# Kernel optimization log

Measured on AMD Instinct MI355X. Metric: run time of the kernel, lower is better.

## Reference

```python
import jax, jax.numpy as jnp
import numpy as np

EPSILON = 0.001
PROXIMITY_THRESHOLD = 0.15


def setup_inputs() -> dict:
    key = jax.random.key(0)
    k1, k2, k3 = jax.random.split(key, 3)
    B, N, E = 8, 512, 4096
    node_positions = jax.random.uniform(k1, (B, N, 2), dtype=jnp.float32)
    adjacency = jax.random.normal(k2, (B, N, N), dtype=jnp.float32)
    edge_index = jax.random.randint(k3, (2, E), 0, B * N, dtype=jnp.int64)
    return {"node_positions": node_positions, "adjacency": adjacency, "edge_index": edge_index}


def _candidate_mask(pos, src, dst, batch, prox):
    # pos: (BN,2); src/dst/batch: (E,)
    p_src = pos[src]
    p_dst = pos[dst]
    mid = (p_src + p_dst) * 0.5                      # (E,2)
    half = jnp.linalg.norm(p_dst - p_src, axis=-1) * 0.5  # (E,)
    dist = jnp.linalg.norm(mid[:, None] - mid[None, :], axis=-1)  # (E,E)
    reach = half[:, None] + half[None, :] + prox
    E = src.shape[0]
    idx = jnp.arange(E)
    upper = idx[None, :] > idx[:, None]              # ei < ej
    same_batch = batch[:, None] == batch[None, :]
    shares = ((src[:, None] == src[None, :]) | (src[:, None] == dst[None, :])
              | (dst[:, None] == src[None, :]) | (dst[:, None] == dst[None, :]))
    return (dist < reach) & upper & same_batch & ~shares


def _segment_distance_dense(p_src, p_dst):
    # All-pairs closest-approach distance between segments i and j.
    d1 = p_dst - p_src                               # (E,2)
    sq = jnp.maximum((d1 * d1).sum(-1), 1e-12)       # (E,)
    a = sq[:, None]                                  # a_i
    e = sq[None, :]                                  # e_j
    b = d1 @ d1.T                                    # (E,E) d1_i . d1_j
    d1_dot_a1 = (d1 * p_src).sum(-1)                 # (E,) d1_k . a1_k
    c = d1_dot_a1[:, None] - d1 @ p_src.T            # d1_i . (a1_i - b1_j)
    f = p_src @ d1.T - d1_dot_a1[None, :]            # d1_j . (a1_i - b1_j)
    denom = jnp.maximum(a * e - b * b, 1e-12)
    s = (b * f - c * e) / denom
    t = (a * f - b * c) / denom
    s = jnp.clip(s, 0.0, 1.0)
    t = jnp.clip(t, 0.0, 1.0)
    t = jnp.clip((b * s + f) / e, 0.0, 1.0)
    s = jnp.clip((b * t - c) / a, 0.0, 1.0)
    closest_a = p_src[:, None, :] + s[..., None] * d1[:, None, :]   # (E,E,2)
    closest_b = p_src[None, :, :] + t[..., None] * d1[None, :, :]   # (E,E,2)
    return jnp.linalg.norm(closest_a - closest_b, axis=-1)          # (E,E)


def reference(node_positions, adjacency, edge_index):
    # adjacency is accepted (per the torch forward signature) but unused by this axiom.
    B, N, _ = node_positions.shape
    pos = node_positions.reshape(-1, 2)              # (B*N, 2)
    src = edge_index[0]
    dst = edge_index[1]
    batch = src // N                                 # (E,) batch membership per edge
    mask = jax.lax.stop_gradient(
        _candidate_mask(jax.lax.stop_gradient(pos), src, dst, batch, PROXIMITY_THRESHOLD))
    dmin = _segment_distance_dense(pos[src], pos[dst])  # (E,E)
    pair_loss = jax.nn.relu(EPSILON - dmin) * mask.astype(dmin.dtype)
    n_pairs = mask.sum()
    loss = pair_loss.sum() / jnp.maximum(n_pairs, 1).astype(dmin.dtype)
    violation_mask = mask & (pair_loss > 0)
    violation_scores = jax.lax.stop_gradient(pair_loss)
    return loss, violation_mask, violation_scores
```

## Files before the change

### kernel.cpp

```cpp
#include <hip/hip_runtime.h>


#define EDGES   4096
#define LOGE    12
#define EPS     0.001f
#define PROX    0.15f
#define NBUCKET 2048

__global__ __launch_bounds__(256) void pair_kernel(
    const float2* __restrict__ pos,
    const int*    __restrict__ esrc,
    const int*    __restrict__ edst,
    float*        __restrict__ out,
    float*        __restrict__ bsum,
    unsigned int* __restrict__ bcnt)
{
#pragma clang fp contract(off)
    const int k = blockIdx.x * 256 + threadIdx.x;
    const int i = k >> LOGE;
    const int j = k & (EDGES - 1);

    const int si = esrc[i], di = edst[i];
    const int sj = esrc[j], dj = edst[j];
    const float2 a1 = pos[si], a2 = pos[di];
    const float2 b1 = pos[sj], b2 = pos[dj];

    const float d1ix = a2.x - a1.x, d1iy = a2.y - a1.y;
    const float d1jx = b2.x - b1.x, d1jy = b2.y - b1.y;
    const float midix = (a1.x + a2.x) * 0.5f, midiy = (a1.y + a2.y) * 0.5f;
    const float midjx = (b1.x + b2.x) * 0.5f, midjy = (b1.y + b2.y) * 0.5f;
    const float half_i = sqrtf(d1ix * d1ix + d1iy * d1iy) * 0.5f;
    const float half_j = sqrtf(d1jx * d1jx + d1jy * d1jy) * 0.5f;
    const float dmx = midix - midjx, dmy = midiy - midjy;
    const float dist  = sqrtf(dmx * dmx + dmy * dmy);
    const float reach = half_i + half_j + PROX;

    const bool upper  = j > i;
    const bool sameb  = (si >> 9) == (sj >> 9);
    const bool shares = (si == sj) || (si == dj) || (di == sj) || (di == dj);
    const bool mask   = (dist < reach) && upper && sameb && !shares;

    const float sqi = fmaxf(d1ix * d1ix + d1iy * d1iy, 1e-12f);
    const float sqj = fmaxf(d1jx * d1jx + d1jy * d1jy, 1e-12f);
    const float b   = d1ix * d1jx + d1iy * d1jy;
    const float ddai = d1ix * a1.x + d1iy * a1.y;
    const float ddaj = d1jx * b1.x + d1jy * b1.y;
    const float c = ddai - (d1ix * b1.x + d1iy * b1.y);
    const float f = (a1.x * d1jx + a1.y * d1jy) - ddaj;
    const float denom = fmaxf(sqi * sqj - b * b, 1e-12f);

    float s = (b * f - c * sqj) / denom;
    s = fminf(fmaxf(s, 0.0f), 1.0f);
    const float t = fminf(fmaxf((b * s + f) / sqj, 0.0f), 1.0f);
    s = fminf(fmaxf((b * t - c) / sqi, 0.0f), 1.0f);

    const float cax = a1.x + s * d1ix, cay = a1.y + s * d1iy;
    const float cbx = b1.x + t * d1jx, cby = b1.y + t * d1jy;
    const float dx = cax - cbx, dy = cay - cby;
    const float dmin = sqrtf(dx * dx + dy * dy);

    const float mf = mask ? 1.0f : 0.0f;
    const float pl = fmaxf(EPS - dmin, 0.0f) * mf;

    out[1 + k] = (mask && pl > 0.0f) ? 1.0f : 0.0f;
    out[1 + EDGES * EDGES + k] = pl;

    float vsum = pl;
    int   vcnt = mask ? 1 : 0;
    #pragma unroll
    for (int off = 32; off > 0; off >>= 1) {
        vsum += __shfl_xor(vsum, off, 64);
        vcnt += __shfl_xor(vcnt, off, 64);
    }
    __shared__ float    ls[4];
    __shared__ unsigned lc[4];
    const int wid = threadIdx.x >> 6, lane = threadIdx.x & 63;
    if (lane == 0) { ls[wid] = vsum; lc[wid] = (unsigned)vcnt; }
    __syncthreads();
    if (threadIdx.x == 0) {
        const float    s4 = ls[0] + ls[1] + ls[2] + ls[3];
        const unsigned c4 = lc[0] + lc[1] + lc[2] + lc[3];
        const int bk = blockIdx.x & (NBUCKET - 1);
        atomicAdd(&bsum[bk], s4);
        atomicAdd(&bcnt[bk], c4);
    }
}

__global__ __launch_bounds__(256) void finalize_kernel(
    const float* __restrict__ bsum, const unsigned* __restrict__ bcnt,
    float* __restrict__ out)
{
    float    s = 0.0f;
    unsigned c = 0u;
    for (int b = threadIdx.x; b < NBUCKET; b += 256) { s += bsum[b]; c += bcnt[b]; }
    #pragma unroll
    for (int off = 32; off > 0; off >>= 1) {
        s += __shfl_xor(s, off, 64);
        c += (unsigned)__shfl_xor((int)c, off, 64);
    }
    __shared__ float    ls[4];
    __shared__ unsigned lc[4];
    const int wid = threadIdx.x >> 6, lane = threadIdx.x & 63;
    if (lane == 0) { ls[wid] = s; lc[wid] = c; }
    __syncthreads();
    if (threadIdx.x == 0) {
        const float    st = ls[0] + ls[1] + ls[2] + ls[3];
        const unsigned ct = lc[0] + lc[1] + lc[2] + lc[3];
        const unsigned n  = ct > 1u ? ct : 1u;
        out[0] = st / (float)n;
    }
}

extern "C" void kernel_launch(void* const* d_in, const int* in_sizes, int n_in,
                              void* d_out, int out_size, void* d_ws, size_t ws_size,
                              hipStream_t stream) {
    const float2* pos  = (const float2*)d_in[0];
    const int*    esrc = (const int*)d_in[2];
    const int*    edst = esrc + EDGES;

    float*        out  = (float*)d_out;
    float*        bsum = (float*)d_ws;
    unsigned int* bcnt = (unsigned int*)((float*)d_ws + NBUCKET);

    hipMemsetAsync(d_ws, 0, NBUCKET * 2 * sizeof(float), stream);

    const int nPairs = EDGES * EDGES;
    pair_kernel<<<nPairs / 256, 256, 0, stream>>>(pos, esrc, edst, out, bsum, bcnt);
    finalize_kernel<<<1, 256, 0, stream>>>(bsum, bcnt, out);
}
```

Measured before the change: 214.9 us.

## Precompute per-edge records and skip lower-triangle pair blocks early

Adds an edge_pre kernel that computes each edge's direction, midpoint, half-length, squared length and dot terms once and packs them into three float4 records. The pair kernel then reads these records instead of doing indirect gathers through edge_index and recomputing per-edge quantities. Blocks that lie entirely in the lower triangle (j <= i) write zeros and return early, and blocks whose partial sum and count are zero skip their atomics. This trades an extra small launch and workspace traffic for much less per-pair arithmetic and gather work. The kernel still has to write the two large output arrays, which likely bounds how much time can be saved.

```diff
diff --git a/kernel.cpp b/kernel.cpp
--- a/kernel.cpp
+++ b/kernel.cpp
@@ -7,46 +7,67 @@
 #define PROX    0.15f
 #define NBUCKET 2048
 
-__global__ __launch_bounds__(256) void pair_kernel(
+__global__ __launch_bounds__(256) void edge_pre(
     const float2* __restrict__ pos,
     const int*    __restrict__ esrc,
     const int*    __restrict__ edst,
+    float4* __restrict__ rec1, float4* __restrict__ rec2, float4* __restrict__ rec3)
+{
+#pragma clang fp contract(off)
+    const int e = blockIdx.x * 256 + threadIdx.x;
+    const int s = esrc[e], d = edst[e];
+    const float2 a1 = pos[s], a2 = pos[d];
+    const float d1x = a2.x - a1.x, d1y = a2.y - a1.y;
+    const float midx = (a1.x + a2.x) * 0.5f, midy = (a1.y + a2.y) * 0.5f;
+    const float half = sqrtf(d1x * d1x + d1y * d1y) * 0.5f;
+    const float sq   = fmaxf(d1x * d1x + d1y * d1y, 1e-12f);
+    const float dda  = d1x * a1.x + d1y * a1.y;
+    rec1[e] = make_float4(a1.x, a1.y, d1x, d1y);
+    rec2[e] = make_float4(midx, midy, half, dda);
+    rec3[e] = make_float4(sq, __int_as_float(s), __int_as_float(d), 0.0f);
+}
+
+__global__ __launch_bounds__(256) void pair_kernel(
+    const float4* __restrict__ rec1, const float4* __restrict__ rec2,
+    const float4* __restrict__ rec3,
     float*        __restrict__ out,
     float*        __restrict__ bsum,
     unsigned int* __restrict__ bcnt)
 {
 #pragma clang fp contract(off)
-    const int k = blockIdx.x * 256 + threadIdx.x;
-    const int i = k >> LOGE;
-    const int j = k & (EDGES - 1);
+    const int bi    = blockIdx.x;
+    const int i     = bi >> 4;
+    const int jbase = (bi & 15) << 8;
+    const int j     = jbase + threadIdx.x;
+    const int k     = (i << LOGE) | j;
 
-    const int si = esrc[i], di = edst[i];
-    const int sj = esrc[j], dj = edst[j];
-    const float2 a1 = pos[si], a2 = pos[di];
-    const float2 b1 = pos[sj], b2 = pos[dj];
+    float* __restrict__ o_mask  = out + 1;
+    float* __restrict__ o_score = out + 1 + EDGES * EDGES;
 
-    const float d1ix = a2.x - a1.x, d1iy = a2.y - a1.y;
-    const float d1jx = b2.x - b1.x, d1jy = b2.y - b1.y;
-    const float midix = (a1.x + a2.x) * 0.5f, midiy = (a1.y + a2.y) * 0.5f;
-    const float midjx = (b1.x + b2.x) * 0.5f, midjy = (b1.y + b2.y) * 0.5f;
-    const float half_i = sqrtf(d1ix * d1ix + d1iy * d1iy) * 0.5f;
-    const float half_j = sqrtf(d1jx * d1jx + d1jy * d1jy) * 0.5f;
-    const float dmx = midix - midjx, dmy = midiy - midjy;
-    const float dist  = sqrtf(dmx * dmx + dmy * dmy);
-    const float reach = half_i + half_j + PROX;
+    if (jbase + 255 <= i) {
+        o_mask[k]  = 0.0f;
+        o_score[k] = 0.0f;
+        return;
+    }
 
+    const float4 r1i = rec1[i], r2i = rec2[i], r3i = rec3[i];
+    const float4 r1j = rec1[j], r2j = rec2[j], r3j = rec3[j];
+
+    const float dmx  = r2i.x - r2j.x, dmy = r2i.y - r2j.y;
+    const float dist = sqrtf(dmx * dmx + dmy * dmy);
+    const float reach = r2i.z + r2j.z + PROX;
+
+    const int si = __float_as_int(r3i.y), di_ = __float_as_int(r3i.z);
+    const int sj = __float_as_int(r3j.y), dj  = __float_as_int(r3j.z);
     const bool upper  = j > i;
     const bool sameb  = (si >> 9) == (sj >> 9);
-    const bool shares = (si == sj) || (si == dj) || (di == sj) || (di == dj);
-    const bool mask   = (dist < reach) && upper && sameb && !shares;
+    const bool shares = (si == sj) | (si == dj) | (di_ == sj) | (di_ == dj);
+    const bool mask   = (dist < reach) & upper & sameb & (!shares);
 
-    const float sqi = fmaxf(d1ix * d1ix + d1iy * d1iy, 1e-12f);
-    const float sqj = fmaxf(d1jx * d1jx + d1jy * d1jy, 1e-12f);
-    const float b   = d1ix * d1jx + d1iy * d1jy;
-    const float ddai = d1ix * a1.x + d1iy * a1.y;
-    const float ddaj = d1jx * b1.x + d1jy * b1.y;
-    const float c = ddai - (d1ix * b1.x + d1iy * b1.y);
-    const float f = (a1.x * d1jx + a1.y * d1jy) - ddaj;
+    const float sqi = r3i.x, sqj = r3j.x;
+    const float b = r1i.z * r1j.z + r1i.w * r1j.w;
+    const float c = r2i.w - (r1i.z * r1j.x + r1i.w * r1j.y);
+    const float f = (r1i.x * r1j.z + r1i.y * r1j.w) - r2j.w;
     const float denom = fmaxf(sqi * sqj - b * b, 1e-12f);
 
     float s = (b * f - c * sqj) / denom;
@@ -54,16 +75,15 @@
     const float t = fminf(fmaxf((b * s + f) / sqj, 0.0f), 1.0f);
     s = fminf(fmaxf((b * t - c) / sqi, 0.0f), 1.0f);
 
-    const float cax = a1.x + s * d1ix, cay = a1.y + s * d1iy;
-    const float cbx = b1.x + t * d1jx, cby = b1.y + t * d1jy;
+    const float cax = r1i.x + s * r1i.z, cay = r1i.y + s * r1i.w;
+    const float cbx = r1j.x + t * r1j.z, cby = r1j.y + t * r1j.w;
     const float dx = cax - cbx, dy = cay - cby;
     const float dmin = sqrtf(dx * dx + dy * dy);
 
-    const float mf = mask ? 1.0f : 0.0f;
-    const float pl = fmaxf(EPS - dmin, 0.0f) * mf;
+    const float pl = fmaxf(EPS - dmin, 0.0f) * (mask ? 1.0f : 0.0f);
 
-    out[1 + k] = (mask && pl > 0.0f) ? 1.0f : 0.0f;
-    out[1 + EDGES * EDGES + k] = pl;
+    o_mask[k]  = (mask && pl > 0.0f) ? 1.0f : 0.0f;
+    o_score[k] = pl;
 
     float vsum = pl;
     int   vcnt = mask ? 1 : 0;
@@ -80,9 +100,11 @@
     if (threadIdx.x == 0) {
         const float    s4 = ls[0] + ls[1] + ls[2] + ls[3];
         const unsigned c4 = lc[0] + lc[1] + lc[2] + lc[3];
-        const int bk = blockIdx.x & (NBUCKET - 1);
-        atomicAdd(&bsum[bk], s4);
-        atomicAdd(&bcnt[bk], c4);
+        if (s4 != 0.0f || c4 != 0u) {
+            const int bk = blockIdx.x & (NBUCKET - 1);
+            atomicAdd(&bsum[bk], s4);
+            atomicAdd(&bcnt[bk], c4);
+        }
     }
 }
 
@@ -121,10 +143,13 @@
     float*        out  = (float*)d_out;
     float*        bsum = (float*)d_ws;
     unsigned int* bcnt = (unsigned int*)((float*)d_ws + NBUCKET);
+    float4*       rec1 = (float4*)((char*)d_ws + NBUCKET * 8);
+    float4*       rec2 = rec1 + EDGES;
+    float4*       rec3 = rec2 + EDGES;
 
     hipMemsetAsync(d_ws, 0, NBUCKET * 2 * sizeof(float), stream);
 
-    const int nPairs = EDGES * EDGES;
-    pair_kernel<<<nPairs / 256, 256, 0, stream>>>(pos, esrc, edst, out, bsum, bcnt);
+    edge_pre<<<EDGES / 256, 256, 0, stream>>>(pos, esrc, edst, rec1, rec2, rec3);
+    pair_kernel<<<(EDGES * EDGES) / 256, 256, 0, stream>>>(rec1, rec2, rec3, out, bsum, bcnt);
     finalize_kernel<<<1, 256, 0, stream>>>(bsum, bcnt, out);
 }
```

Measured after the change: 191.7 us. 1.12x faster.
